# Kernel tuning notes

Measured on AMD Instinct MI355X. Metric: run time of the kernel, lower is better.

## Reference

```python
import jax, jax.numpy as jnp
import numpy as np

B, H, W, C = 32, 32, 32, 256


def setup_inputs() -> dict:
    key = jax.random.key(0)
    k1, k2 = jax.random.split(key)
    feats1 = jax.random.normal(k1, (B, H, W, C), dtype=jnp.float32)
    feats2 = jax.random.normal(k2, (B, H, W, C), dtype=jnp.float32)
    return {"feats1": feats1, "feats2": feats2}


def reference(feats1, feats2):
    # Training path of LocalFeatureLoss (trainflag=True)
    b, h, w, c = feats1.shape
    l = h * w
    q = feats1.reshape(b, l, c)  # queries: (B, l, C)
    p = feats2.reshape(b, l, c)  # preds:   (B, l, C)
    # M[b, a, j] = <p[b,a], q[b,j]>  == fm2 @ fm1.T per batch
    M = jnp.einsum('bac,bjc->baj', p, q)  # (B, l_pred, l_query)
    max1 = jnp.argmax(M, axis=1)  # (B, l_q): best pred index for each query token
    max2 = jnp.argmax(M, axis=2)  # (B, l_p): best query index for each pred token
    # mutual nearest-neighbor check: m[b, j] = max2[b, max1[b, j]]
    m = jnp.take_along_axis(max2, max1, axis=1)  # (B, l_q)
    valid = jnp.arange(l)[None, :] == m          # (B, l_q) bool
    # gather matched pred descriptors and compute per-pair similarity
    matched_p = jnp.take_along_axis(p, max1[..., None], axis=1)  # (B, l_q, C)
    sims = jnp.sum(q * matched_p, axis=-1)                        # (B, l_q)
    cnt = jnp.sum(valid, axis=1).astype(sims.dtype)               # (B,)
    # mean over mutual NN pairs (torch mean over idx1)
    similarity = jnp.sum(jnp.where(valid, sims, 0.0), axis=1) / jnp.maximum(cnt, 1.0)
    return similarity
```

## Files before the change

kernel.cpp:

```cpp
#include <hip/hip_runtime.h>
#include <hip/hip_bf16.h>

#define BATCH 32
#define L 1024
#define CD 256
#define BM 128
#define BN 128
#define BK 64
#define NRT (L / BM)
#define NCT (L / BN)
#define TILE_E 8192

typedef __bf16 bf16x8 __attribute__((ext_vector_type(8)));
typedef float  f32x4  __attribute__((ext_vector_type(4)));
typedef unsigned long long u64;

__device__ __forceinline__ unsigned int enc_f32(float f) {
    unsigned int u = __float_as_uint(f);
    return ((int)u < 0) ? ~u : (u | 0x80000000u);
}
__device__ __forceinline__ float dec_f32(unsigned int u) {
    u = (u & 0x80000000u) ? (u & 0x7FFFFFFFu) : ~u;
    return __uint_as_float(u);
}
__device__ __forceinline__ u64 pmax(u64 a, u64 b) { return a > b ? a : b; }

__device__ __forceinline__ void gl_lds16(const __bf16* g, __bf16* l) {
    __builtin_amdgcn_global_load_lds(
        (const __attribute__((address_space(1))) unsigned int*)g,
        (__attribute__((address_space(3))) unsigned int*)l, 16, 0, 0);
}

__global__ __launch_bounds__(256) void convert_kernel(
    const float* __restrict__ qg,
    const float* __restrict__ pg,
    __bf16* __restrict__ qsw,
    __bf16* __restrict__ psw)
{
    const unsigned int t = blockIdx.x * 256 + threadIdx.x;
    const unsigned int v = t & ((1u << 20) - 1);
    const bool isQ = (t >> 20) != 0;
    const float* src_base = isQ ? qg : pg;
    __bf16*      dst_base = isQ ? qsw : psw;

    const int s    = v & 7;
    const int row  = (v >> 3) & 127;
    const int step = (v >> 10) & 3;
    const int pan  = (v >> 12) & 7;
    const int b    = v >> 15;

    const float* src = src_base
        + ((size_t)b * L + pan * 128 + row) * CD
        + step * 64 + ((s ^ (row & 7)) * 8);
    const float4 f0 = *(const float4*)src;
    const float4 f1 = *(const float4*)(src + 4);
    bf16x8 o;
    o[0] = (__bf16)f0.x; o[1] = (__bf16)f0.y; o[2] = (__bf16)f0.z; o[3] = (__bf16)f0.w;
    o[4] = (__bf16)f1.x; o[5] = (__bf16)f1.y; o[6] = (__bf16)f1.z; o[7] = (__bf16)f1.w;
    *(bf16x8*)&dst_base[(size_t)v * 8] = o;
}

__global__ __launch_bounds__(512) void mm_argmax_kernel(
    const __bf16* __restrict__ qsw,
    const __bf16* __restrict__ psw,
    u64* __restrict__ colpart,
    u64* __restrict__ rowpart)
{
    __shared__ __bf16 sA[4][TILE_E];
    __shared__ __bf16 sB[4][TILE_E];
    __shared__ u64 sRow[2][BM];
    __shared__ u64 sCol[4][BN];

    const int tid = threadIdx.x;
    const int bid = blockIdx.x;
    const int b    = bid & 31;
    const int tile = bid >> 5;
    const int rt   = tile >> 3;
    const int ct   = tile & 7;
    const int row0 = rt * BM;
    const int col0 = ct * BN;

    const int lane = tid & 63;
    const int w    = tid >> 6;
    const int wm   = w >> 1;
    const int wn   = w & 1;
    const int quad = lane >> 4;
    const int l16  = lane & 15;

    const __bf16* pa = psw + (size_t)(b * 8 + rt) * 4 * TILE_E;
    const __bf16* pb = qsw + (size_t)(b * 8 + ct) * 4 * TILE_E;

    #pragma unroll
    for (int s = 0; s < 4; ++s) {
        gl_lds16(pa + s * TILE_E +        tid * 8, &sA[s][tid * 8]);
        gl_lds16(pa + s * TILE_E + 4096 + tid * 8, &sA[s][4096 + tid * 8]);
        gl_lds16(pb + s * TILE_E +        tid * 8, &sB[s][tid * 8]);
        gl_lds16(pb + s * TILE_E + 4096 + tid * 8, &sB[s][4096 + tid * 8]);
    }

    f32x4 acc[2][4];
    #pragma unroll
    for (int tm = 0; tm < 2; ++tm)
        #pragma unroll
        for (int tn = 0; tn < 4; ++tn) acc[tm][tn] = (f32x4){0.f, 0.f, 0.f, 0.f};

    #define STEP_SYNC(N)                                           \
        asm volatile("s_waitcnt vmcnt(" #N ")" ::: "memory");      \
        __builtin_amdgcn_s_barrier();                              \
        __builtin_amdgcn_sched_barrier(0);

    #define COMPUTE(s)                                                         \
        __builtin_amdgcn_s_setprio(1);                                         \
        _Pragma("unroll")                                                      \
        for (int kk = 0; kk < 2; ++kk) {                                       \
            const int sw = ((kk * 4 + quad) ^ (l16 & 7)) << 3;                 \
            bf16x8 a0 = *(const bf16x8*)&sA[s][(wm * 32      + l16) * BK + sw]; \
            bf16x8 a1 = *(const bf16x8*)&sA[s][(wm * 32 + 16 + l16) * BK + sw]; \
            bf16x8 b0 = *(const bf16x8*)&sB[s][(wn * 64      + l16) * BK + sw]; \
            bf16x8 b1 = *(const bf16x8*)&sB[s][(wn * 64 + 16 + l16) * BK + sw]; \
            bf16x8 b2 = *(const bf16x8*)&sB[s][(wn * 64 + 32 + l16) * BK + sw]; \
            bf16x8 b3 = *(const bf16x8*)&sB[s][(wn * 64 + 48 + l16) * BK + sw]; \
            acc[0][0] = __builtin_amdgcn_mfma_f32_16x16x32_bf16(a0, b0, acc[0][0], 0, 0, 0); \
            acc[0][1] = __builtin_amdgcn_mfma_f32_16x16x32_bf16(a0, b1, acc[0][1], 0, 0, 0); \
            acc[0][2] = __builtin_amdgcn_mfma_f32_16x16x32_bf16(a0, b2, acc[0][2], 0, 0, 0); \
            acc[0][3] = __builtin_amdgcn_mfma_f32_16x16x32_bf16(a0, b3, acc[0][3], 0, 0, 0); \
            acc[1][0] = __builtin_amdgcn_mfma_f32_16x16x32_bf16(a1, b0, acc[1][0], 0, 0, 0); \
            acc[1][1] = __builtin_amdgcn_mfma_f32_16x16x32_bf16(a1, b1, acc[1][1], 0, 0, 0); \
            acc[1][2] = __builtin_amdgcn_mfma_f32_16x16x32_bf16(a1, b2, acc[1][2], 0, 0, 0); \
            acc[1][3] = __builtin_amdgcn_mfma_f32_16x16x32_bf16(a1, b3, acc[1][3], 0, 0, 0); \
        }                                                                      \
        __builtin_amdgcn_s_setprio(0);

    STEP_SYNC(12) COMPUTE(0)
    STEP_SYNC(8)  COMPUTE(1)
    STEP_SYNC(4)  COMPUTE(2)
    STEP_SYNC(0)  COMPUTE(3)

    #undef STEP_SYNC
    #undef COMPUTE

    const int a_base = row0 + wm * 32 + quad * 4;
    const int j_base = col0 + wn * 64 + l16;

    #pragma unroll
    for (int tn = 0; tn < 4; ++tn) {
        float cv = acc[0][tn][0];
        int   ca = a_base;
        #pragma unroll
        for (int tm = 0; tm < 2; ++tm)
            #pragma unroll
            for (int r = 0; r < 4; ++r) {
                if (tm == 0 && r == 0) continue;
                const float v = acc[tm][tn][r];
                const int   a = a_base + tm * 16 + r;
                if (v > cv) { cv = v; ca = a; }
            }
        u64 pk = ((u64)enc_f32(cv) << 32) | (unsigned int)(~(unsigned int)ca);
        pk = pmax(pk, __shfl_xor(pk, 16));
        pk = pmax(pk, __shfl_xor(pk, 32));
        if (quad == 0) sCol[wm][wn * 64 + tn * 16 + l16] = pk;
    }

    #pragma unroll
    for (int tm = 0; tm < 2; ++tm)
        #pragma unroll
        for (int r = 0; r < 4; ++r) {
            float rv = acc[tm][0][r];
            int   rj = j_base;
            #pragma unroll
            for (int tn = 1; tn < 4; ++tn) {
                const float v = acc[tm][tn][r];
                if (v > rv) { rv = v; rj = j_base + tn * 16; }
            }
            u64 pk = ((u64)enc_f32(rv) << 32) | (unsigned int)(~(unsigned int)rj);
            pk = pmax(pk, __shfl_xor(pk, 1));
            pk = pmax(pk, __shfl_xor(pk, 2));
            pk = pmax(pk, __shfl_xor(pk, 4));
            pk = pmax(pk, __shfl_xor(pk, 8));
            if (l16 == 0) sRow[wn][wm * 32 + tm * 16 + quad * 4 + r] = pk;
        }

    __syncthreads();
    if (tid < BN) {
        u64 c = pmax(pmax(sCol[0][tid], sCol[1][tid]),
                     pmax(sCol[2][tid], sCol[3][tid]));
        colpart[((size_t)b * NRT + rt) * L + col0 + tid] = c;
        u64 rr = pmax(sRow[0][tid], sRow[1][tid]);
        rowpart[((size_t)b * NCT + ct) * L + row0 + tid] = rr;
    }
}

__global__ __launch_bounds__(1024) void finalize_kernel(
    const u64* __restrict__ colpart,
    const u64* __restrict__ rowpart,
    float* __restrict__ out)
{
    __shared__ int sMax2[L];
    __shared__ float sSum[16];
    __shared__ int sCnt[16];
    const int b = blockIdx.x;
    const int j = threadIdx.x;

    u64 rb = 0ull;
    #pragma unroll
    for (int ct = 0; ct < NCT; ++ct)
        rb = pmax(rb, rowpart[((size_t)b * NCT + ct) * L + j]);
    sMax2[j] = (int)(~(unsigned int)rb) & (L - 1);

    u64 cb = 0ull;
    #pragma unroll
    for (int rt = 0; rt < NRT; ++rt)
        cb = pmax(cb, colpart[((size_t)b * NRT + rt) * L + j]);
    __syncthreads();

    const int a = (int)(~(unsigned int)cb) & (L - 1);
    const float val = dec_f32((unsigned int)(cb >> 32));
    const bool mut = (sMax2[a] == j);
    float sum = mut ? val : 0.f;
    int   cnt = mut ? 1 : 0;

    #pragma unroll
    for (int o = 32; o >= 1; o >>= 1) {
        sum += __shfl_down(sum, o);
        cnt += __shfl_down(cnt, o);
    }
    if ((j & 63) == 0) { sSum[j >> 6] = sum; sCnt[j >> 6] = cnt; }
    __syncthreads();
    if (j == 0) {
        float S = 0.f;
        int   C = 0;
        #pragma unroll
        for (int i = 0; i < 16; ++i) { S += sSum[i]; C += sCnt[i]; }
        out[b] = S / fmaxf((float)C, 1.0f);
    }
}

extern "C" void kernel_launch(void* const* d_in, const int* in_sizes, int n_in,
                              void* d_out, int out_size, void* d_ws, size_t ws_size,
                              hipStream_t stream) {
    const float* q = (const float*)d_in[0];
    const float* p = (const float*)d_in[1];
    float* out = (float*)d_out;

    u64* colpart = (u64*)d_ws;
    u64* rowpart = colpart + (size_t)BATCH * NRT * L;
    __bf16* psw = (__bf16*)(rowpart + (size_t)BATCH * NCT * L);
    __bf16* qsw = psw + (size_t)BATCH * 8 * 4 * TILE_E;

    convert_kernel<<<8192, 256, 0, stream>>>(q, p, qsw, psw);
    mm_argmax_kernel<<<BATCH * NRT * NCT, 512, 0, stream>>>(qsw, psw, colpart, rowpart);
    finalize_kernel<<<BATCH, 1024, 0, stream>>>(colpart, rowpart, out);
}
```

Measured before the change: 150.8 us.

## Make each block own a row panel and stream column tiles with double buffering

Each matmul block now keeps a 128-row panel of p resident in LDS and loops over 16 column tiles of q (64 columns each), double-buffering the B tiles with async global-to-LDS loads. Row argmax is accumulated in registers across the whole column loop, so max2 is written directly and the rowpart reduction in finalize goes away. Column partials are written per wave (32 per batch) instead of per block. The grid shrinks from 2048 blocks to 256, which may leave CUs underused, and LDS per block grows to about 128KB.

```diff
diff --git a/kernel.cpp b/kernel.cpp
--- a/kernel.cpp
+++ b/kernel.cpp
@@ -4,12 +4,10 @@
 #define BATCH 32
 #define L 1024
 #define CD 256
-#define BM 128
-#define BN 128
-#define BK 64
-#define NRT (L / BM)
-#define NCT (L / BN)
-#define TILE_E 8192
+#define NRT 8
+#define NCT 16
+#define PAN_A 32768
+#define TILE_B 16384
 
 typedef __bf16 bf16x8 __attribute__((ext_vector_type(8)));
 typedef float  f32x4  __attribute__((ext_vector_type(4)));
@@ -40,45 +38,50 @@
     const unsigned int t = blockIdx.x * 256 + threadIdx.x;
     const unsigned int v = t & ((1u << 20) - 1);
     const bool isQ = (t >> 20) != 0;
-    const float* src_base = isQ ? qg : pg;
-    __bf16*      dst_base = isQ ? qsw : psw;
-
-    const int s    = v & 7;
-    const int row  = (v >> 3) & 127;
-    const int step = (v >> 10) & 3;
-    const int pan  = (v >> 12) & 7;
-    const int b    = v >> 15;
-
-    const float* src = src_base
-        + ((size_t)b * L + pan * 128 + row) * CD
-        + step * 64 + ((s ^ (row & 7)) * 8);
+
+    const float* src;
+    __bf16* dst;
+    if (isQ) {
+        const int s    = v & 7;
+        const int row  = (v >> 3) & 63;
+        const int step = (v >> 9) & 3;
+        const int ct   = (v >> 11) & 15;
+        const int b    = v >> 15;
+        src = qg + ((size_t)(b * L + ct * 64 + row)) * CD
+                 + step * 64 + ((s ^ (row & 7)) * 8);
+        dst = qsw + (size_t)v * 8;
+    } else {
+        const int s    = v & 7;
+        const int row  = (v >> 3) & 127;
+        const int step = (v >> 10) & 3;
+        const int pan  = (v >> 12) & 7;
+        const int b    = v >> 15;
+        src = pg + ((size_t)(b * L + pan * 128 + row)) * CD
+                 + step * 64 + ((s ^ (row & 7)) * 8);
+        dst = psw + (size_t)v * 8;
+    }
     const float4 f0 = *(const float4*)src;
     const float4 f1 = *(const float4*)(src + 4);
     bf16x8 o;
     o[0] = (__bf16)f0.x; o[1] = (__bf16)f0.y; o[2] = (__bf16)f0.z; o[3] = (__bf16)f0.w;
     o[4] = (__bf16)f1.x; o[5] = (__bf16)f1.y; o[6] = (__bf16)f1.z; o[7] = (__bf16)f1.w;
-    *(bf16x8*)&dst_base[(size_t)v * 8] = o;
-}
-
-__global__ __launch_bounds__(512) void mm_argmax_kernel(
+    *(bf16x8*)&dst[0] = o;
+}
+
+__global__ __launch_bounds__(512, 2) void mm_argmax_kernel(
     const __bf16* __restrict__ qsw,
     const __bf16* __restrict__ psw,
     u64* __restrict__ colpart,
-    u64* __restrict__ rowpart)
+    int* __restrict__ max2)
 {
-    __shared__ __bf16 sA[4][TILE_E];
-    __shared__ __bf16 sB[4][TILE_E];
-    __shared__ u64 sRow[2][BM];
-    __shared__ u64 sCol[4][BN];
+    __shared__ __bf16 sA[4 * 8192];
+    __shared__ __bf16 sB[2][4 * 4096];
+    __shared__ u64 sRow[2][128];
 
     const int tid = threadIdx.x;
     const int bid = blockIdx.x;
-    const int b    = bid & 31;
-    const int tile = bid >> 5;
-    const int rt   = tile >> 3;
-    const int ct   = tile & 7;
-    const int row0 = rt * BM;
-    const int col0 = ct * BN;
+    const int b  = bid & 31;
+    const int rt = bid >> 5;
 
     const int lane = tid & 63;
     const int w    = tid >> 6;
@@ -87,112 +90,124 @@
     const int quad = lane >> 4;
     const int l16  = lane & 15;
 
-    const __bf16* pa = psw + (size_t)(b * 8 + rt) * 4 * TILE_E;
-    const __bf16* pb = qsw + (size_t)(b * 8 + ct) * 4 * TILE_E;
-
-    #pragma unroll
-    for (int s = 0; s < 4; ++s) {
-        gl_lds16(pa + s * TILE_E +        tid * 8, &sA[s][tid * 8]);
-        gl_lds16(pa + s * TILE_E + 4096 + tid * 8, &sA[s][4096 + tid * 8]);
-        gl_lds16(pb + s * TILE_E +        tid * 8, &sB[s][tid * 8]);
-        gl_lds16(pb + s * TILE_E + 4096 + tid * 8, &sB[s][4096 + tid * 8]);
-    }
-
-    f32x4 acc[2][4];
+    const __bf16* pa  = psw + (size_t)(b * NRT + rt) * PAN_A;
+    const __bf16* pbb = qsw + (size_t)b * NCT * TILE_B;
+
+    #pragma unroll
+    for (int c = 0; c < 8; ++c)
+        gl_lds16(pa + c * 4096 + tid * 8, &sA[c * 4096 + tid * 8]);
+    #pragma unroll
+    for (int c = 0; c < 4; ++c)
+        gl_lds16(pbb + c * 4096 + tid * 8, &sB[0][c * 4096 + tid * 8]);
+    #pragma unroll
+    for (int c = 0; c < 4; ++c)
+        gl_lds16(pbb + TILE_B + c * 4096 + tid * 8, &sB[1][c * 4096 + tid * 8]);
+
+    f32x4 acc[2][2];
+    float rowv[2][4];
+    int   rowj[2][4];
     #pragma unroll
     for (int tm = 0; tm < 2; ++tm)
         #pragma unroll
-        for (int tn = 0; tn < 4; ++tn) acc[tm][tn] = (f32x4){0.f, 0.f, 0.f, 0.f};
-
-    #define STEP_SYNC(N)                                           \
-        asm volatile("s_waitcnt vmcnt(" #N ")" ::: "memory");      \
-        __builtin_amdgcn_s_barrier();                              \
+        for (int r = 0; r < 4; ++r) { rowv[tm][r] = -1e30f; rowj[tm][r] = 0; }
+
+    asm volatile("s_waitcnt vmcnt(4)" ::: "memory");
+    __builtin_amdgcn_s_barrier();
+    __builtin_amdgcn_sched_barrier(0);
+
+    const size_t colbase = ((size_t)(b * NRT + rt) * 4 + wm) * L;
+    const int a0q = rt * 128 + wm * 32 + quad * 4;
+
+    for (int t = 0; t < NCT; ++t) {
+        const __bf16* sBb = sB[t & 1];
+        #pragma unroll
+        for (int tm = 0; tm < 2; ++tm)
+            #pragma unroll
+            for (int tn = 0; tn < 2; ++tn) acc[tm][tn] = (f32x4){0.f, 0.f, 0.f, 0.f};
+
+        __builtin_amdgcn_s_setprio(1);
+        #pragma unroll
+        for (int step = 0; step < 4; ++step) {
+            #pragma unroll
+            for (int kk = 0; kk < 2; ++kk) {
+                const int sw = ((kk * 4 + quad) ^ (l16 & 7)) << 3;
+                bf16x8 a0 = *(const bf16x8*)&sA [step * 8192 + (wm * 32      + l16) * 64 + sw];
+                bf16x8 a1 = *(const bf16x8*)&sA [step * 8192 + (wm * 32 + 16 + l16) * 64 + sw];
+                bf16x8 b0 = *(const bf16x8*)&sBb[step * 4096 + (wn * 32      + l16) * 64 + sw];
+                bf16x8 b1 = *(const bf16x8*)&sBb[step * 4096 + (wn * 32 + 16 + l16) * 64 + sw];
+                acc[0][0] = __builtin_amdgcn_mfma_f32_16x16x32_bf16(a0, b0, acc[0][0], 0, 0, 0);
+                acc[0][1] = __builtin_amdgcn_mfma_f32_16x16x32_bf16(a0, b1, acc[0][1], 0, 0, 0);
+                acc[1][0] = __builtin_amdgcn_mfma_f32_16x16x32_bf16(a1, b0, acc[1][0], 0, 0, 0);
+                acc[1][1] = __builtin_amdgcn_mfma_f32_16x16x32_bf16(a1, b1, acc[1][1], 0, 0, 0);
+            }
+        }
+        __builtin_amdgcn_s_setprio(0);
+
+        const int jb = t * 64 + wn * 32 + l16;
+        #pragma unroll
+        for (int tm = 0; tm < 2; ++tm)
+            #pragma unroll
+            for (int r = 0; r < 4; ++r) {
+                const float v0 = acc[tm][0][r], v1 = acc[tm][1][r];
+                if (v0 > rowv[tm][r]) { rowv[tm][r] = v0; rowj[tm][r] = jb; }
+                if (v1 > rowv[tm][r]) { rowv[tm][r] = v1; rowj[tm][r] = jb + 16; }
+            }
+
+        #pragma unroll
+        for (int tn = 0; tn < 2; ++tn) {
+            float cv = acc[0][tn][0];
+            int   ca = a0q;
+            #pragma unroll
+            for (int r = 1; r < 4; ++r)
+                if (acc[0][tn][r] > cv) { cv = acc[0][tn][r]; ca = a0q + r; }
+            #pragma unroll
+            for (int r = 0; r < 4; ++r)
+                if (acc[1][tn][r] > cv) { cv = acc[1][tn][r]; ca = a0q + 16 + r; }
+            u64 pk = ((u64)enc_f32(cv) << 32) | (unsigned int)(~(unsigned int)ca);
+            pk = pmax(pk, __shfl_xor(pk, 16));
+            pk = pmax(pk, __shfl_xor(pk, 32));
+            if (quad == 0)
+                colpart[colbase + t * 64 + wn * 32 + tn * 16 + l16] = pk;
+        }
+
+        __builtin_amdgcn_s_barrier();
         __builtin_amdgcn_sched_barrier(0);
-
-    #define COMPUTE(s)                                                         \
-        __builtin_amdgcn_s_setprio(1);                                         \
-        _Pragma("unroll")                                                      \
-        for (int kk = 0; kk < 2; ++kk) {                                       \
-            const int sw = ((kk * 4 + quad) ^ (l16 & 7)) << 3;                 \
-            bf16x8 a0 = *(const bf16x8*)&sA[s][(wm * 32      + l16) * BK + sw]; \
-            bf16x8 a1 = *(const bf16x8*)&sA[s][(wm * 32 + 16 + l16) * BK + sw]; \
-            bf16x8 b0 = *(const bf16x8*)&sB[s][(wn * 64      + l16) * BK + sw]; \
-            bf16x8 b1 = *(const bf16x8*)&sB[s][(wn * 64 + 16 + l16) * BK + sw]; \
-            bf16x8 b2 = *(const bf16x8*)&sB[s][(wn * 64 + 32 + l16) * BK + sw]; \
-            bf16x8 b3 = *(const bf16x8*)&sB[s][(wn * 64 + 48 + l16) * BK + sw]; \
-            acc[0][0] = __builtin_amdgcn_mfma_f32_16x16x32_bf16(a0, b0, acc[0][0], 0, 0, 0); \
-            acc[0][1] = __builtin_amdgcn_mfma_f32_16x16x32_bf16(a0, b1, acc[0][1], 0, 0, 0); \
-            acc[0][2] = __builtin_amdgcn_mfma_f32_16x16x32_bf16(a0, b2, acc[0][2], 0, 0, 0); \
-            acc[0][3] = __builtin_amdgcn_mfma_f32_16x16x32_bf16(a0, b3, acc[0][3], 0, 0, 0); \
-            acc[1][0] = __builtin_amdgcn_mfma_f32_16x16x32_bf16(a1, b0, acc[1][0], 0, 0, 0); \
-            acc[1][1] = __builtin_amdgcn_mfma_f32_16x16x32_bf16(a1, b1, acc[1][1], 0, 0, 0); \
-            acc[1][2] = __builtin_amdgcn_mfma_f32_16x16x32_bf16(a1, b2, acc[1][2], 0, 0, 0); \
-            acc[1][3] = __builtin_amdgcn_mfma_f32_16x16x32_bf16(a1, b3, acc[1][3], 0, 0, 0); \
-        }                                                                      \
-        __builtin_amdgcn_s_setprio(0);
-
-    STEP_SYNC(12) COMPUTE(0)
-    STEP_SYNC(8)  COMPUTE(1)
-    STEP_SYNC(4)  COMPUTE(2)
-    STEP_SYNC(0)  COMPUTE(3)
-
-    #undef STEP_SYNC
-    #undef COMPUTE
-
-    const int a_base = row0 + wm * 32 + quad * 4;
-    const int j_base = col0 + wn * 64 + l16;
-
-    #pragma unroll
-    for (int tn = 0; tn < 4; ++tn) {
-        float cv = acc[0][tn][0];
-        int   ca = a_base;
-        #pragma unroll
-        for (int tm = 0; tm < 2; ++tm)
-            #pragma unroll
-            for (int r = 0; r < 4; ++r) {
-                if (tm == 0 && r == 0) continue;
-                const float v = acc[tm][tn][r];
-                const int   a = a_base + tm * 16 + r;
-                if (v > cv) { cv = v; ca = a; }
-            }
-        u64 pk = ((u64)enc_f32(cv) << 32) | (unsigned int)(~(unsigned int)ca);
-        pk = pmax(pk, __shfl_xor(pk, 16));
-        pk = pmax(pk, __shfl_xor(pk, 32));
-        if (quad == 0) sCol[wm][wn * 64 + tn * 16 + l16] = pk;
+        if (t + 2 < NCT) {
+            #pragma unroll
+            for (int c = 0; c < 4; ++c)
+                gl_lds16(pbb + (size_t)(t + 2) * TILE_B + c * 4096 + tid * 8,
+                         &sB[t & 1][c * 4096 + tid * 8]);
+        }
+        if (t < NCT - 1) {
+            if (t + 2 < NCT) { asm volatile("s_waitcnt vmcnt(6)" ::: "memory"); }
+            else             { asm volatile("s_waitcnt vmcnt(2)" ::: "memory"); }
+            __builtin_amdgcn_s_barrier();
+            __builtin_amdgcn_sched_barrier(0);
+        }
     }
 
     #pragma unroll
     for (int tm = 0; tm < 2; ++tm)
         #pragma unroll
         for (int r = 0; r < 4; ++r) {
-            float rv = acc[tm][0][r];
-            int   rj = j_base;
-            #pragma unroll
-            for (int tn = 1; tn < 4; ++tn) {
-                const float v = acc[tm][tn][r];
-                if (v > rv) { rv = v; rj = j_base + tn * 16; }
-            }
-            u64 pk = ((u64)enc_f32(rv) << 32) | (unsigned int)(~(unsigned int)rj);
+            u64 pk = ((u64)enc_f32(rowv[tm][r]) << 32)
+                   | (unsigned int)(~(unsigned int)rowj[tm][r]);
             pk = pmax(pk, __shfl_xor(pk, 1));
             pk = pmax(pk, __shfl_xor(pk, 2));
             pk = pmax(pk, __shfl_xor(pk, 4));
             pk = pmax(pk, __shfl_xor(pk, 8));
             if (l16 == 0) sRow[wn][wm * 32 + tm * 16 + quad * 4 + r] = pk;
         }
-
     __syncthreads();
-    if (tid < BN) {
-        u64 c = pmax(pmax(sCol[0][tid], sCol[1][tid]),
-                     pmax(sCol[2][tid], sCol[3][tid]));
-        colpart[((size_t)b * NRT + rt) * L + col0 + tid] = c;
-        u64 rr = pmax(sRow[0][tid], sRow[1][tid]);
-        rowpart[((size_t)b * NCT + ct) * L + row0 + tid] = rr;
+    if (tid < 128) {
+        const u64 m = pmax(sRow[0][tid], sRow[1][tid]);
+        max2[(size_t)b * L + rt * 128 + tid] = (int)(~(unsigned int)m) & (L - 1);
     }
 }
 
 __global__ __launch_bounds__(1024) void finalize_kernel(
     const u64* __restrict__ colpart,
-    const u64* __restrict__ rowpart,
+    const int* __restrict__ max2,
     float* __restrict__ out)
 {
     __shared__ int sMax2[L];
@@ -201,16 +216,12 @@
     const int b = blockIdx.x;
     const int j = threadIdx.x;
 
-    u64 rb = 0ull;
-    #pragma unroll
-    for (int ct = 0; ct < NCT; ++ct)
-        rb = pmax(rb, rowpart[((size_t)b * NCT + ct) * L + j]);
-    sMax2[j] = (int)(~(unsigned int)rb) & (L - 1);
+    sMax2[j] = max2[(size_t)b * L + j];
 
     u64 cb = 0ull;
     #pragma unroll
-    for (int rt = 0; rt < NRT; ++rt)
-        cb = pmax(cb, colpart[((size_t)b * NRT + rt) * L + j]);
+    for (int k = 0; k < 32; ++k)
+        cb = pmax(cb, colpart[((size_t)b * 32 + k) * L + j]);
     __syncthreads();
 
     const int a = (int)(~(unsigned int)cb) & (L - 1);
@@ -243,11 +254,11 @@
     float* out = (float*)d_out;
 
     u64* colpart = (u64*)d_ws;
-    u64* rowpart = colpart + (size_t)BATCH * NRT * L;
-    __bf16* psw = (__bf16*)(rowpart + (size_t)BATCH * NCT * L);
-    __bf16* qsw = psw + (size_t)BATCH * 8 * 4 * TILE_E;
+    int* max2 = (int*)(colpart + (size_t)BATCH * 32 * L);
+    __bf16* psw = (__bf16*)((char*)d_ws + 8 * 1024 * 1024 + 512 * 1024);
+    __bf16* qsw = psw + (size_t)BATCH * NRT * PAN_A;
 
     convert_kernel<<<8192, 256, 0, stream>>>(q, p, qsw, psw);
-    mm_argmax_kernel<<<BATCH * NRT * NCT, 512, 0, stream>>>(qsw, psw, colpart, rowpart);
-    finalize_kernel<<<BATCH, 1024, 0, stream>>>(colpart, rowpart, out);
-}
+    mm_argmax_kernel<<<BATCH * NRT, 512, 0, stream>>>(qsw, psw, colpart, max2);
+    finalize_kernel<<<BATCH, 1024, 0, stream>>>(colpart, max2, out);
+}
```

Measured after the change: 141.0 us. 6.5% less time.
